# Kernel optimization log

Measured on AMD Instinct MI355X. Metric: run time of the kernel, lower is better.

Reference implementation:

```python
import jax, jax.numpy as jnp
import numpy as np

# Bernstein-basis theta coefficients for d=2 (calculate_theta2(2)),
# inv_coeff order: [x^0, x^1, x^2]
THETAS = ((3.0, -3.0, 0.75), (0.0, 3.0, -1.5), (0.0, 0.0, 0.75))
HIGH_ORDER = 2

N_NODES = 50000
N_EDGES = 800000
IN_DIM, HID_DIM, OUT_DIM = 128, 64, 2


def setup_inputs() -> dict:
    key = jax.random.key(0)
    ks = jax.random.split(key, 16)
    f32 = jnp.float32
    def w(k, shape, fan_in):
        return jax.random.normal(k, shape, dtype=f32) * (1.0 / np.sqrt(fan_in))
    return {
        "in_feat": jax.random.normal(ks[0], (N_NODES, IN_DIM), dtype=f32),
        "src": jax.random.randint(ks[1], (N_EDGES,), 0, N_NODES, dtype=jnp.int32),
        "dst": jax.random.randint(ks[2], (N_EDGES,), 0, N_NODES, dtype=jnp.int32),
        "W1": w(ks[3], (IN_DIM, HID_DIM), IN_DIM), "b1": jnp.zeros((HID_DIM,), f32),
        "W2": w(ks[4], (HID_DIM, HID_DIM), HID_DIM), "b2": jnp.zeros((HID_DIM,), f32),
        "W3": w(ks[5], (HID_DIM * 5, HID_DIM), HID_DIM * 5), "b3": jnp.zeros((HID_DIM,), f32),
        "W4": w(ks[6], (HID_DIM, OUT_DIM), HID_DIM), "b4": jnp.zeros((OUT_DIM,), f32),
        "Wg1": w(ks[7], (IN_DIM, HID_DIM), IN_DIM), "bg1": jnp.zeros((HID_DIM,), f32),
        "Wg2": w(ks[8], (HID_DIM, IN_DIM), HID_DIM), "bg2": jnp.zeros((IN_DIM,), f32),
    }


def _spmm(x, src, dst, n):
    # y[v] = sum_{(u,v) in E} x[u]   (DGL update_all(copy_u, sum))
    return jax.ops.segment_sum(x[src], dst, num_segments=n)


def reference(in_feat, src, dst, W1, b1, W2, b2, W3, b3, W4, b4, Wg1, bg1, Wg2, bg2):
    n = in_feat.shape[0]
    ones_e = jnp.ones(src.shape[0], dtype=in_feat.dtype)
    deg_in = jnp.clip(jax.ops.segment_sum(ones_e, dst, num_segments=n), 1.0)
    deg_out = jnp.clip(jax.ops.segment_sum(ones_e, src, num_segments=n), 1.0)
    din = (deg_in ** -0.5)[:, None]   # [N,1]
    dout = (deg_out ** -0.5)[:, None]

    def lap(f):
        # f - D^{-1/2} A D^{-1/2} f  (in-degree norm, as in unnLaplacian)
        return f - _spmm(f * din, src, dst, n) * din

    # MLP front-end
    h = jax.nn.relu(in_feat @ W1 + b1)
    h = jax.nn.relu(h @ W2 + b2)

    branches = []
    # BandConv branches (lin=False): theta-weighted Laplacian polynomial
    for theta in THETAS:
        f = h
        acc = theta[0] * h
        for k in range(1, len(theta)):
            f = lap(f)
            acc = acc + theta[k] * f
        branches.append(acc)
    # HighConv branches: repeated Laplacian, num_layer = 1..HIGH_ORDER
    f = h
    for j in range(HIGH_ORDER):
        f = lap(f)
        branches.append(f)

    h_final = jnp.concatenate(branches, axis=-1)  # [N, 5*hid]
    out = jax.nn.relu(h_final @ W3 + b3) @ W4 + b4  # [N, out_dim]

    # GCN branch on self-loop-free graph (same edges here): symmetric norm GraphConv
    def gconv(x, W, b):
        return _spmm(x * dout, src, dst, n) * din @ W + b
    emb = gconv(jax.nn.relu(gconv(in_feat, Wg1, bg1)), Wg2, bg2)  # [N, in_dim]

    return out, emb
```

## Files before the change

kernel.cpp:

```cpp
#include <hip/hip_runtime.h>
#include <hip/hip_bf16.h>
#include <math.h>

#define NN 50000
#define NE 800000
#define C128 128
#define CE 6250
#define NR 8
#define RNOD 6250
#define RW 3125
#define NW 25000
#define HISTB 1024
#define INITB 96
#define RB 98
#define GB 782
#define ZSB 782
#define FSG 3125

typedef _Float16 half8 __attribute__((ext_vector_type(8)));
typedef float f32x4 __attribute__((ext_vector_type(4)));
typedef unsigned short ushort4v __attribute__((ext_vector_type(4)));

static inline int cdiv(int a, int b) { return (a + b - 1) / b; }


__device__ inline size_t pack_pos(int k, int n, int K, int M) {
    int tile = n >> 4;
    int kstep = k >> 5;
    int quad = (k >> 3) & 3;
    int j = k & 7;
    int lane = (quad << 4) | (n & 15);
    return ((size_t)(tile * (K >> 5) + kstep) * 64 + lane) * 8 + j;
}

__device__ void pack_std_dev(int bx, const float* __restrict__ W, _Float16* __restrict__ Wpk,
                             int K, int M) {
    int idx = bx * 256 + threadIdx.x;
    if (idx >= K * M) return;
    int k = idx / M, n = idx % M;
    Wpk[pack_pos(k, n, K, M)] = (_Float16)W[idx];
}

__device__ void pack_wc_dev(int bx, const float* __restrict__ W3, _Float16* __restrict__ wcpk) {
    int idx = bx * 256 + threadIdx.x;
    if (idx >= 3 * 4096) return;
    int b = idx >> 12;
    int rem = idx & 4095;
    int k = rem >> 6, n = rem & 63;
    float w0 = W3[(0 * 64 + k) * 64 + n];
    float w1 = W3[(1 * 64 + k) * 64 + n];
    float w2 = W3[(2 * 64 + k) * 64 + n];
    float w3 = W3[(3 * 64 + k) * 64 + n];
    float w4 = W3[(4 * 64 + k) * 64 + n];
    float v;
    if (b == 0)      v = 3.f * w0;
    else if (b == 1) v = -3.f * w0 + 3.f * w1 + w3;
    else             v = 0.75f * w0 - 1.5f * w1 + 0.75f * w2 + w4;
    wcpk[pack_pos(b * 64 + k, n, 192, 64)] = (_Float16)v;
}

__device__ void init_dev(int bx,
                         const float* __restrict__ W2, _Float16* __restrict__ W2pk,
                         const float* __restrict__ Wg2, _Float16* __restrict__ Wg2pk,
                         const float* __restrict__ W3, _Float16* __restrict__ wcpk) {
    if (bx < 16) { pack_std_dev(bx, W2, W2pk, 64, 64); return; }
    bx -= 16;
    if (bx < 32) { pack_std_dev(bx, Wg2, Wg2pk, 64, 128); return; }
    bx -= 32;
    pack_wc_dev(bx, W3, wcpk);
}


__device__ void hist_dev(int bx, const int* __restrict__ idx, unsigned* __restrict__ H,
                         unsigned* __restrict__ cnt) {
    int c = bx & 127, r = bx >> 7;
    int tid = threadIdx.x;
    for (int j = tid; j < RW; j += 256) cnt[j] = 0;
    __syncthreads();
    int lo = r * RNOD;
    const int* p = idx + (size_t)c * CE;
    for (int i = tid; i < CE; i += 256) {
        int v = p[i] - lo;
        if ((unsigned)v < (unsigned)RNOD)
            atomicAdd(&cnt[v >> 1], 1u << ((v & 1) * 16));
    }
    __syncthreads();
    unsigned* outp = H + (size_t)c * NW + r * RW;
    for (int j = tid; j < RW; j += 256) outp[j] = cnt[j];
}

__device__ void reduce_dev(int bx, const unsigned* __restrict__ H, int* __restrict__ dgo,
                           float* __restrict__ o_rsq, float* __restrict__ o_inv,
                           float* __restrict__ o_sq) {
    int w = bx * 256 + threadIdx.x;
    if (w >= NW) return;
    unsigned slo = 0, shi = 0;
#pragma unroll 8
    for (int c = 0; c < C128; c++) {
        unsigned h = H[(size_t)c * NW + w];
        slo += h & 0xffffu; shi += h >> 16;
    }
    if (dgo) {
        dgo[2 * w]     = slo > 64u ? 64 : (int)slo;
        dgo[2 * w + 1] = shi > 64u ? 64 : (int)shi;
    }
    float f0 = (float)(slo < 1u ? 1u : slo);
    float f1 = (float)(shi < 1u ? 1u : shi);
    o_rsq[2 * w] = rsqrtf(f0); o_rsq[2 * w + 1] = rsqrtf(f1);
    if (o_inv) { o_inv[2 * w] = 1.f / f0; o_inv[2 * w + 1] = 1.f / f1; }
    if (o_sq)  { o_sq[2 * w] = sqrtf(f0); o_sq[2 * w + 1] = sqrtf(f1); }
}

__device__ void prefix_dev(int bx, const unsigned* __restrict__ HD, unsigned* __restrict__ baseD) {
    int w = bx * 256 + threadIdx.x;
    if (w >= NW) return;
    unsigned slo = 0, shi = 0;
#pragma unroll 8
    for (int c = 0; c < C128; c++) {
        unsigned b0 = slo > 64u ? 64u : slo;
        unsigned b1 = shi > 64u ? 64u : shi;
        baseD[(size_t)c * NW + w] = b0 | (b1 << 16);
        unsigned h = HD[(size_t)c * NW + w];
        slo += h & 0xffffu; shi += h >> 16;
    }
}

__device__ void scatter_dev(int bx, const int* __restrict__ src, const int* __restrict__ dst,
                            const unsigned* __restrict__ baseD,
                            unsigned short* __restrict__ colsPad,
                            unsigned* __restrict__ cnt) {
    int c = bx & 127, r = bx >> 7;
    int tid = threadIdx.x;
    const unsigned* bslice = baseD + (size_t)c * NW + r * RW;
    for (int j = tid; j < RW; j += 256) cnt[j] = bslice[j];
    __syncthreads();
    int lo = r * RNOD;
    const int* pd = dst + (size_t)c * CE;
    const int* ps = src + (size_t)c * CE;
    for (int i = tid; i < CE; i += 256) {
        int v = pd[i];
        int lv = v - lo;
        if ((unsigned)lv < (unsigned)RNOD) {
            int sh = (lv & 1) * 16;
            unsigned old = atomicAdd(&cnt[lv >> 1], 1u << sh);
            unsigned pos = (old >> sh) & 0xffffu;
            if (pos < 64u) colsPad[(size_t)v * 64 + pos] = (unsigned short)ps[i];
        }
    }
}

__device__ void zscale_dev(int bx, half8* __restrict__ pair, const float* __restrict__ dout, int N) {
    int idx = bx * 256 + threadIdx.x;
    if (idx >= N * 4) return;
    int row = idx >> 2, q = idx & 3;
    float m = dout[row];
    half8* z = pair + (size_t)row * 16 + 8 + q * 2;
    half8 a = z[0], b = z[1];
#pragma unroll
    for (int j = 0; j < 8; j++) {
        a[j] = (_Float16)((float)a[j] * m);
        b[j] = (_Float16)((float)b[j] * m);
    }
    z[0] = a; z[1] = b;
}


struct HSegs { const _Float16* p[3]; int ld[3]; };

template <int M, int K, bool OUTW, bool RSCA>
__device__ void mg_dev(int bx, HSegs A, const half8* __restrict__ Wpk,
                       const float* __restrict__ bias, int relu,
                       float* __restrict__ C,
                       _Float16* __restrict__ Ch0, const float* __restrict__ ms0,
                       const float* __restrict__ rsc,
                       const float* __restrict__ W4, const float* __restrict__ b4,
                       float* __restrict__ outp, int ldC, int N) {
    constexpr int NT = M / 16;
    constexpr int NKS = K / 32;
    int tid = threadIdx.x;
    int wave = tid >> 6, lane = tid & 63;
    int quad = lane >> 4, m = lane & 15;
    int row0 = bx * 64 + wave * 16;
    int rowA = row0 + m; if (rowA >= N) rowA = N - 1;
    _Float16 hs = (_Float16)1.f;
    if (RSCA) hs = (_Float16)rsc[rowA];
    f32x4 acc[NT];
#pragma unroll
    for (int t = 0; t < NT; t++) acc[t] = (f32x4){0.f, 0.f, 0.f, 0.f};
#pragma unroll
    for (int ks = 0; ks < NKS; ks++) {
        const _Float16* ap = A.p[ks >> 1] + (size_t)rowA * A.ld[ks >> 1] + (ks & 1) * 32 + quad * 8;
        half8 af = *(const half8*)ap;
        if (RSCA) {
#pragma unroll
            for (int j = 0; j < 8; j++) af[j] *= hs;
        }
#pragma unroll
        for (int t = 0; t < NT; t++) {
            half8 bf = Wpk[(t * NKS + ks) * 64 + lane];
            acc[t] = __builtin_amdgcn_mfma_f32_16x16x32_f16(af, bf, acc[t], 0, 0, 0);
        }
    }
    float outv[NT][4];
#pragma unroll
    for (int t = 0; t < NT; t++) {
        float bv = bias ? bias[t * 16 + m] : 0.f;
#pragma unroll
        for (int r = 0; r < 4; r++) {
            float v = acc[t][r] + bv;
            if (relu) v = fmaxf(v, 0.f);
            outv[t][r] = v;
        }
    }
    if (OUTW) {
        float w40[NT], w41[NT];
#pragma unroll
        for (int t = 0; t < NT; t++) {
            w40[t] = W4[(t * 16 + m) * 2];
            w41[t] = W4[(t * 16 + m) * 2 + 1];
        }
#pragma unroll
        for (int r = 0; r < 4; r++) {
            float p0 = 0.f, p1 = 0.f;
#pragma unroll
            for (int t = 0; t < NT; t++) {
                p0 += outv[t][r] * w40[t];
                p1 += outv[t][r] * w41[t];
            }
#pragma unroll
            for (int off = 1; off < 16; off <<= 1) {
                p0 += __shfl_xor(p0, off);
                p1 += __shfl_xor(p1, off);
            }
            int row = row0 + quad * 4 + r;
            if (m == 0 && row < N) {
                outp[(size_t)row * 2 + 0] = p0 + b4[0];
                outp[(size_t)row * 2 + 1] = p1 + b4[1];
            }
        }
    }
    if (C || Ch0) {
#pragma unroll
        for (int r = 0; r < 4; r++) {
            int row = row0 + quad * 4 + r;
            if (row >= N) continue;
            float m0 = (Ch0 && ms0) ? ms0[row] : 1.f;
#pragma unroll
            for (int t = 0; t < NT; t++) {
                size_t off = (size_t)row * ldC + t * 16 + m;
                if (C)   C[off] = outv[t][r];
                if (Ch0) Ch0[off] = (_Float16)(outv[t][r] * m0);
            }
        }
    }
}

__device__ void a15_dev(int bx, const float* __restrict__ in_feat,
                        const float* __restrict__ W1, const float* __restrict__ Wg1,
                        const float* __restrict__ b1,
                        _Float16* __restrict__ h1h, _Float16* __restrict__ zh,
                        _Float16* __restrict__ wsm, int N) {
    int tid = threadIdx.x;
    int wave = tid >> 6, lane = tid & 63;
    int quad = lane >> 4, m = lane & 15;
    int row0 = bx * 64 + wave * 16;
    int rowA = row0 + m; if (rowA >= N) rowA = N - 1;
    half8 af[4];
#pragma unroll
    for (int ks = 0; ks < 4; ks++) {
        const float* ap = in_feat + (size_t)rowA * 128 + ks * 32 + quad * 8;
        float4 u = *(const float4*)ap;
        float4 v = *(const float4*)(ap + 4);
        af[ks][0] = (_Float16)u.x; af[ks][1] = (_Float16)u.y;
        af[ks][2] = (_Float16)u.z; af[ks][3] = (_Float16)u.w;
        af[ks][4] = (_Float16)v.x; af[ks][5] = (_Float16)v.y;
        af[ks][6] = (_Float16)v.z; af[ks][7] = (_Float16)v.w;
    }
    const half8* wf = (const half8*)wsm;
    f32x4 acc[4];
    for (int i = tid; i < 8192; i += 256)
        wsm[pack_pos(i >> 6, i & 63, 128, 64)] = (_Float16)W1[i];
    __syncthreads();
#pragma unroll
    for (int t = 0; t < 4; t++) acc[t] = (f32x4){0.f, 0.f, 0.f, 0.f};
#pragma unroll
    for (int ks = 0; ks < 4; ks++)
#pragma unroll
        for (int t = 0; t < 4; t++)
            acc[t] = __builtin_amdgcn_mfma_f32_16x16x32_f16(af[ks], wf[(t * 4 + ks) * 64 + lane], acc[t], 0, 0, 0);
#pragma unroll
    for (int r = 0; r < 4; r++) {
        int row = row0 + quad * 4 + r;
        if (row >= N) continue;
#pragma unroll
        for (int t = 0; t < 4; t++)
            h1h[(size_t)row * 64 + t * 16 + m] = (_Float16)fmaxf(acc[t][r] + b1[t * 16 + m], 0.f);
    }
    __syncthreads();
    for (int i = tid; i < 8192; i += 256)
        wsm[pack_pos(i >> 6, i & 63, 128, 64)] = (_Float16)Wg1[i];
    __syncthreads();
#pragma unroll
    for (int t = 0; t < 4; t++) acc[t] = (f32x4){0.f, 0.f, 0.f, 0.f};
#pragma unroll
    for (int ks = 0; ks < 4; ks++)
#pragma unroll
        for (int t = 0; t < 4; t++)
            acc[t] = __builtin_amdgcn_mfma_f32_16x16x32_f16(af[ks], wf[(t * 4 + ks) * 64 + lane], acc[t], 0, 0, 0);
#pragma unroll
    for (int r = 0; r < 4; r++) {
        int row = row0 + quad * 4 + r;
        if (row >= N) continue;
#pragma unroll
        for (int t = 0; t < 4; t++)
            zh[(size_t)row * 128 + t * 16 + m] = (_Float16)acc[t][r];
    }
}


__launch_bounds__(256)
__global__ void k_L1(const float* __restrict__ in_feat,
                     const float* __restrict__ W1, const float* __restrict__ Wg1,
                     const float* __restrict__ b1,
                     _Float16* __restrict__ h1h, _Float16* __restrict__ zh,
                     const float* __restrict__ W2, _Float16* __restrict__ W2pk,
                     const float* __restrict__ Wg2, _Float16* __restrict__ Wg2pk,
                     const float* __restrict__ W3, _Float16* __restrict__ wcpk,
                     const int* __restrict__ src, const int* __restrict__ dst,
                     unsigned* __restrict__ HD, unsigned* __restrict__ HS, int N) {
    __shared__ _Float16 smh[8192];
    int bx = blockIdx.x;
    if (bx < GB) { a15_dev(bx, in_feat, W1, Wg1, b1, h1h, zh, smh, N); return; }
    bx -= GB;
    if (bx < INITB) { init_dev(bx, W2, W2pk, Wg2, Wg2pk, W3, wcpk); return; }
    bx -= INITB;
    if (bx < HISTB) { hist_dev(bx, dst, HD, (unsigned*)smh); return; }
    bx -= HISTB;
    hist_dev(bx, src, HS, (unsigned*)smh);
}

__launch_bounds__(256)
__global__ void k_L2(const unsigned* __restrict__ HD, const unsigned* __restrict__ HS,
                     int* __restrict__ degin, float* __restrict__ din,
                     float* __restrict__ din2, float* __restrict__ dsq,
                     float* __restrict__ dout, unsigned* __restrict__ baseD) {
    int bx = blockIdx.x;
    if (bx < RB) { reduce_dev(bx, HD, degin, din, din2, dsq); return; }
    bx -= RB;
    if (bx < RB) { reduce_dev(bx, HS, nullptr, dout, nullptr, nullptr); return; }
    bx -= RB;
    prefix_dev(bx, HD, baseD);
}

__launch_bounds__(256)
__global__ void k_L3(const int* __restrict__ src, const int* __restrict__ dst,
                     const unsigned* __restrict__ baseD, unsigned short* __restrict__ colsPad,
                     const _Float16* __restrict__ h1h, const half8* __restrict__ W2pk,
                     const float* __restrict__ b2, _Float16* __restrict__ pair0h,
                     const float* __restrict__ din,
                     half8* __restrict__ pair0v, const float* __restrict__ dout, int N) {
    __shared__ unsigned cnt[RW];
    int bx = blockIdx.x;
    if (bx < HISTB) { scatter_dev(bx, src, dst, baseD, colsPad, cnt); return; }
    bx -= HISTB;
    if (bx < GB) {
        HSegs A;
        A.p[0] = h1h; A.ld[0] = 64;
        A.p[1] = nullptr; A.ld[1] = 0;
        A.p[2] = nullptr; A.ld[2] = 0;
        mg_dev<64, 64, false, false>(bx, A, W2pk, b2, 1, nullptr, pair0h, din,
                                     nullptr, nullptr, nullptr, nullptr, 128, N);
        return;
    }
    bx -= GB;
    zscale_dev(bx, pair0v, dout, N);
}


struct FSP {
    const half8* xp;
    half8* uOut; int uld;
    half8* zOut; int zld;
    const float* din2;
    const float* zrs1;
    const float* bgz;
    const float* zrs2;
    int zrelu;
};

__launch_bounds__(256)
__global__ void k_FS(FSP P, const unsigned short* __restrict__ colsPad,
                     const int* __restrict__ deg, int N) {
    int g = blockIdx.x;
    int tid = threadIdx.x;
    int wave = tid >> 6, lane = tid & 63;
    int grp = lane >> 4, c = lane & 15;
    int row = g * 16 + wave * 4 + grp;
    if (row >= N) return;
    int dg = deg[row];
    const unsigned short* cp = colsPad + (size_t)row * 64;
    float acc[8];
#pragma unroll
    for (int j = 0; j < 8; j++) acc[j] = 0.f;
    int e = 0;
    for (; e + 7 < dg; e += 8) {
        ushort4v sa = *(const ushort4v*)(cp + e);
        ushort4v sb = *(const ushort4v*)(cp + e + 4);
        half8 v0 = P.xp[(size_t)sa.x * 16 + c];
        half8 v1 = P.xp[(size_t)sa.y * 16 + c];
        half8 v2 = P.xp[(size_t)sa.z * 16 + c];
        half8 v3 = P.xp[(size_t)sa.w * 16 + c];
        half8 v4 = P.xp[(size_t)sb.x * 16 + c];
        half8 v5 = P.xp[(size_t)sb.y * 16 + c];
        half8 v6 = P.xp[(size_t)sb.z * 16 + c];
        half8 v7 = P.xp[(size_t)sb.w * 16 + c];
#pragma unroll
        for (int j = 0; j < 8; j++) {
            acc[j] += (float)v0[j] + (float)v1[j] + (float)v2[j] + (float)v3[j]
                    + (float)v4[j] + (float)v5[j] + (float)v6[j] + (float)v7[j];
        }
    }
    for (; e + 3 < dg; e += 4) {
        ushort4v ss = *(const ushort4v*)(cp + e);
        half8 v0 = P.xp[(size_t)ss.x * 16 + c];
        half8 v1 = P.xp[(size_t)ss.y * 16 + c];
        half8 v2 = P.xp[(size_t)ss.z * 16 + c];
        half8 v3 = P.xp[(size_t)ss.w * 16 + c];
#pragma unroll
        for (int j = 0; j < 8; j++)
            acc[j] += (float)v0[j] + (float)v1[j] + (float)v2[j] + (float)v3[j];
    }
    for (; e < dg; e++) {
        int s = cp[e];
        half8 v = P.xp[(size_t)s * 16 + c];
#pragma unroll
        for (int j = 0; j < 8; j++) acc[j] += (float)v[j];
    }
    half8 h;
    if (c < 8) {
        float d = P.din2[row];
        half8 f = P.xp[(size_t)row * 16 + c];
#pragma unroll
        for (int j = 0; j < 8; j++)
            h[j] = (_Float16)((float)f[j] - acc[j] * d);
        P.uOut[(size_t)row * P.uld + c] = h;
    } else {
        float s1 = P.zrs1[row];
#pragma unroll
        for (int j = 0; j < 8; j++) acc[j] *= s1;
        if (P.bgz) {
            const float* bb = P.bgz + (c - 8) * 8;
#pragma unroll
            for (int j = 0; j < 8; j++) acc[j] += bb[j];
        }
        if (P.zrelu) {
#pragma unroll
            for (int j = 0; j < 8; j++) acc[j] = fmaxf(acc[j], 0.f);
        }
        float s2 = P.zrs2 ? P.zrs2[row] : 1.f;
#pragma unroll
        for (int j = 0; j < 8; j++) h[j] = (_Float16)(acc[j] * s2);
        P.zOut[(size_t)row * P.zld + (c - 8)] = h;
    }
}

__launch_bounds__(256)
__global__ void k_F3(const _Float16* __restrict__ pair0, const _Float16* __restrict__ pair1,
                     const _Float16* __restrict__ u2h, const half8* __restrict__ wcpk,
                     const float* __restrict__ b3, const float* __restrict__ dsq,
                     const float* __restrict__ W4, const float* __restrict__ b4,
                     float* __restrict__ outp,
                     const _Float16* __restrict__ sgh, const half8* __restrict__ Wg2pk,
                     const float* __restrict__ bg2, float* __restrict__ emb, int N) {
    int bx = blockIdx.x;
    if (bx < GB) {
        HSegs A;
        A.p[0] = pair0; A.ld[0] = 128;
        A.p[1] = pair1; A.ld[1] = 128;
        A.p[2] = u2h;   A.ld[2] = 64;
        mg_dev<64, 192, true, true>(bx, A, wcpk, b3, 1, nullptr, nullptr, nullptr,
                                    dsq, W4, b4, outp, 64, N);
        return;
    }
    bx -= GB;
    HSegs A;
    A.p[0] = sgh; A.ld[0] = 64;
    A.p[1] = nullptr; A.ld[1] = 0;
    A.p[2] = nullptr; A.ld[2] = 0;
    mg_dev<128, 64, false, false>(bx, A, Wg2pk, bg2, 0, emb, nullptr, nullptr,
                                  nullptr, nullptr, nullptr, nullptr, 128, N);
}

extern "C" void kernel_launch(void* const* d_in, const int* in_sizes, int n_in,
                              void* d_out, int out_size, void* d_ws, size_t ws_size,
                              hipStream_t stream) {
    const int N = NN;
    const float* in_feat = (const float*)d_in[0];
    const int* src = (const int*)d_in[1];
    const int* dst = (const int*)d_in[2];
    const float* W1 = (const float*)d_in[3];
    const float* b1 = (const float*)d_in[4];
    const float* W2 = (const float*)d_in[5];
    const float* b2 = (const float*)d_in[6];
    const float* W3 = (const float*)d_in[7];
    const float* b3 = (const float*)d_in[8];
    const float* W4 = (const float*)d_in[9];
    const float* b4 = (const float*)d_in[10];
    const float* Wg1 = (const float*)d_in[11];
    const float* bg1 = (const float*)d_in[12];
    const float* Wg2 = (const float*)d_in[13];
    const float* bg2 = (const float*)d_in[14];

    float* out = (float*)d_out;
    float* emb = out + (size_t)N * 2;

    float* fw = (float*)d_ws;
    float* din  = fw;
    float* din2 = din + N;
    float* dsq  = din2 + N;
    float* dout = dsq + N;
    int* degin  = (int*)(dout + N);
    unsigned short* colsPad = (unsigned short*)(degin + N);
    unsigned* HD   = (unsigned*)(colsPad + (size_t)64 * N);
    unsigned* HS   = HD + (size_t)C128 * NW;
    unsigned* baseD = HS + (size_t)C128 * NW;
    _Float16* hp = (_Float16*)(baseD + (size_t)C128 * NW);
    _Float16* h1h   = hp;
    _Float16* pair0 = h1h + (size_t)64 * N;
    _Float16* pair1 = pair0 + (size_t)128 * N;
    _Float16* u2h   = pair1 + (size_t)128 * N;
    _Float16* sgh   = u2h + (size_t)64 * N;
    _Float16* W2pk  = sgh + (size_t)64 * N;
    _Float16* Wg2pk = W2pk + 4096;
    _Float16* wcpk  = Wg2pk + 8192;

    k_L1<<<GB + INITB + 2 * HISTB, 256, 0, stream>>>(in_feat, W1, Wg1, b1,
        h1h, pair0 + 64, W2, W2pk, Wg2, Wg2pk, W3, wcpk, src, dst, HD, HS, N);

    k_L2<<<3 * RB, 256, 0, stream>>>(HD, HS, degin, din, din2, dsq, dout, baseD);

    k_L3<<<HISTB + GB + ZSB, 256, 0, stream>>>(src, dst, baseD, colsPad,
        h1h, (const half8*)W2pk, b2, pair0, din, (half8*)pair0, dout, N);

    FSP p;
    p = {(const half8*)pair0, (half8*)pair1, 16, (half8*)pair1 + 8, 16,
         din2, din, bg1, dout, 1};
    k_FS<<<FSG, 256, 0, stream>>>(p, colsPad, degin, N);

    p = {(const half8*)pair1, (half8*)u2h, 8, (half8*)sgh, 8,
         din2, din, nullptr, nullptr, 0};
    k_FS<<<FSG, 256, 0, stream>>>(p, colsPad, degin, N);

    k_F3<<<2 * GB, 256, 0, stream>>>(pair0, pair1, u2h, (const half8*)wcpk, b3, dsq,
        W4, b4, out, sgh, (const half8*)Wg2pk, bg2, emb, N);
}
```

Baseline: 248.3 us.

## Vectorize edge index loads and merge in-degree reduce into prefix pass

Histogram and scatter loops now read edge indices as int2 pairs, halving load instructions. The separate in-degree reduction pass, which re-read the full HD histogram, is merged into the prefix pass, so HD is scanned once instead of twice. Weight-packing blocks move from the first launch into the second, freeing the first kernel for histogram and GEMM work. The int2 loads assume the per-chunk base pointers are 8-byte aligned, which holds because CE is even.

```diff
diff --git a/kernel.cpp b/kernel.cpp
--- a/kernel.cpp
+++ b/kernel.cpp
@@ -78,20 +78,22 @@
     for (int j = tid; j < RW; j += 256) cnt[j] = 0;
     __syncthreads();
     int lo = r * RNOD;
-    const int* p = idx + (size_t)c * CE;
-    for (int i = tid; i < CE; i += 256) {
-        int v = p[i] - lo;
-        if ((unsigned)v < (unsigned)RNOD)
-            atomicAdd(&cnt[v >> 1], 1u << ((v & 1) * 16));
+    const int2* p2 = (const int2*)(idx + (size_t)c * CE);
+    for (int i = tid; i < CE / 2; i += 256) {
+        int2 e = p2[i];
+        int v0 = e.x - lo, v1 = e.y - lo;
+        if ((unsigned)v0 < (unsigned)RNOD)
+            atomicAdd(&cnt[v0 >> 1], 1u << ((v0 & 1) * 16));
+        if ((unsigned)v1 < (unsigned)RNOD)
+            atomicAdd(&cnt[v1 >> 1], 1u << ((v1 & 1) * 16));
     }
     __syncthreads();
     unsigned* outp = H + (size_t)c * NW + r * RW;
     for (int j = tid; j < RW; j += 256) outp[j] = cnt[j];
 }
 
-__device__ void reduce_dev(int bx, const unsigned* __restrict__ H, int* __restrict__ dgo,
-                           float* __restrict__ o_rsq, float* __restrict__ o_inv,
-                           float* __restrict__ o_sq) {
+__device__ void reduce_dev(int bx, const unsigned* __restrict__ H,
+                           float* __restrict__ o_rsq) {
     int w = bx * 256 + threadIdx.x;
     if (w >= NW) return;
     unsigned slo = 0, shi = 0;
@@ -100,18 +102,15 @@
         unsigned h = H[(size_t)c * NW + w];
         slo += h & 0xffffu; shi += h >> 16;
     }
-    if (dgo) {
-        dgo[2 * w]     = slo > 64u ? 64 : (int)slo;
-        dgo[2 * w + 1] = shi > 64u ? 64 : (int)shi;
-    }
     float f0 = (float)(slo < 1u ? 1u : slo);
     float f1 = (float)(shi < 1u ? 1u : shi);
     o_rsq[2 * w] = rsqrtf(f0); o_rsq[2 * w + 1] = rsqrtf(f1);
-    if (o_inv) { o_inv[2 * w] = 1.f / f0; o_inv[2 * w + 1] = 1.f / f1; }
-    if (o_sq)  { o_sq[2 * w] = sqrtf(f0); o_sq[2 * w + 1] = sqrtf(f1); }
-}
-
-__device__ void prefix_dev(int bx, const unsigned* __restrict__ HD, unsigned* __restrict__ baseD) {
+}
+
+__device__ void prefnorm_dev(int bx, const unsigned* __restrict__ HD,
+                             unsigned* __restrict__ baseD,
+                             int* __restrict__ dgo, float* __restrict__ o_rsq,
+                             float* __restrict__ o_inv, float* __restrict__ o_sq) {
     int w = bx * 256 + threadIdx.x;
     if (w >= NW) return;
     unsigned slo = 0, shi = 0;
@@ -123,6 +122,13 @@
         unsigned h = HD[(size_t)c * NW + w];
         slo += h & 0xffffu; shi += h >> 16;
     }
+    dgo[2 * w]     = slo > 64u ? 64 : (int)slo;
+    dgo[2 * w + 1] = shi > 64u ? 64 : (int)shi;
+    float f0 = (float)(slo < 1u ? 1u : slo);
+    float f1 = (float)(shi < 1u ? 1u : shi);
+    o_rsq[2 * w] = rsqrtf(f0); o_rsq[2 * w + 1] = rsqrtf(f1);
+    o_inv[2 * w] = 1.f / f0;   o_inv[2 * w + 1] = 1.f / f1;
+    o_sq[2 * w] = sqrtf(f0);   o_sq[2 * w + 1] = sqrtf(f1);
 }
 
 __device__ void scatter_dev(int bx, const int* __restrict__ src, const int* __restrict__ dst,
@@ -135,16 +141,24 @@
     for (int j = tid; j < RW; j += 256) cnt[j] = bslice[j];
     __syncthreads();
     int lo = r * RNOD;
-    const int* pd = dst + (size_t)c * CE;
-    const int* ps = src + (size_t)c * CE;
-    for (int i = tid; i < CE; i += 256) {
-        int v = pd[i];
-        int lv = v - lo;
-        if ((unsigned)lv < (unsigned)RNOD) {
-            int sh = (lv & 1) * 16;
-            unsigned old = atomicAdd(&cnt[lv >> 1], 1u << sh);
+    const int2* pd2 = (const int2*)(dst + (size_t)c * CE);
+    const int2* ps2 = (const int2*)(src + (size_t)c * CE);
+    for (int i = tid; i < CE / 2; i += 256) {
+        int2 ed = pd2[i];
+        int2 es = ps2[i];
+        int lv0 = ed.x - lo;
+        if ((unsigned)lv0 < (unsigned)RNOD) {
+            int sh = (lv0 & 1) * 16;
+            unsigned old = atomicAdd(&cnt[lv0 >> 1], 1u << sh);
             unsigned pos = (old >> sh) & 0xffffu;
-            if (pos < 64u) colsPad[(size_t)v * 64 + pos] = (unsigned short)ps[i];
+            if (pos < 64u) colsPad[(size_t)ed.x * 64 + pos] = (unsigned short)es.x;
+        }
+        int lv1 = ed.y - lo;
+        if ((unsigned)lv1 < (unsigned)RNOD) {
+            int sh = (lv1 & 1) * 16;
+            unsigned old = atomicAdd(&cnt[lv1 >> 1], 1u << sh);
+            unsigned pos = (old >> sh) & 0xffffu;
+            if (pos < 64u) colsPad[(size_t)ed.y * 64 + pos] = (unsigned short)es.y;
         }
     }
 }
@@ -323,17 +337,12 @@
                      const float* __restrict__ W1, const float* __restrict__ Wg1,
                      const float* __restrict__ b1,
                      _Float16* __restrict__ h1h, _Float16* __restrict__ zh,
-                     const float* __restrict__ W2, _Float16* __restrict__ W2pk,
-                     const float* __restrict__ Wg2, _Float16* __restrict__ Wg2pk,
-                     const float* __restrict__ W3, _Float16* __restrict__ wcpk,
                      const int* __restrict__ src, const int* __restrict__ dst,
                      unsigned* __restrict__ HD, unsigned* __restrict__ HS, int N) {
     __shared__ _Float16 smh[8192];
     int bx = blockIdx.x;
     if (bx < GB) { a15_dev(bx, in_feat, W1, Wg1, b1, h1h, zh, smh, N); return; }
     bx -= GB;
-    if (bx < INITB) { init_dev(bx, W2, W2pk, Wg2, Wg2pk, W3, wcpk); return; }
-    bx -= INITB;
     if (bx < HISTB) { hist_dev(bx, dst, HD, (unsigned*)smh); return; }
     bx -= HISTB;
     hist_dev(bx, src, HS, (unsigned*)smh);
@@ -343,13 +352,16 @@
 __global__ void k_L2(const unsigned* __restrict__ HD, const unsigned* __restrict__ HS,
                      int* __restrict__ degin, float* __restrict__ din,
                      float* __restrict__ din2, float* __restrict__ dsq,
-                     float* __restrict__ dout, unsigned* __restrict__ baseD) {
+                     float* __restrict__ dout, unsigned* __restrict__ baseD,
+                     const float* __restrict__ W2, _Float16* __restrict__ W2pk,
+                     const float* __restrict__ Wg2, _Float16* __restrict__ Wg2pk,
+                     const float* __restrict__ W3, _Float16* __restrict__ wcpk) {
     int bx = blockIdx.x;
-    if (bx < RB) { reduce_dev(bx, HD, degin, din, din2, dsq); return; }
+    if (bx < RB) { reduce_dev(bx, HS, dout); return; }
     bx -= RB;
-    if (bx < RB) { reduce_dev(bx, HS, nullptr, dout, nullptr, nullptr); return; }
+    if (bx < RB) { prefnorm_dev(bx, HD, baseD, degin, din, din2, dsq); return; }
     bx -= RB;
-    prefix_dev(bx, HD, baseD);
+    init_dev(bx, W2, W2pk, Wg2, Wg2pk, W3, wcpk);
 }
 
 __launch_bounds__(256)
@@ -534,10 +546,11 @@
     _Float16* Wg2pk = W2pk + 4096;
     _Float16* wcpk  = Wg2pk + 8192;
 
-    k_L1<<<GB + INITB + 2 * HISTB, 256, 0, stream>>>(in_feat, W1, Wg1, b1,
-        h1h, pair0 + 64, W2, W2pk, Wg2, Wg2pk, W3, wcpk, src, dst, HD, HS, N);
-
-    k_L2<<<3 * RB, 256, 0, stream>>>(HD, HS, degin, din, din2, dsq, dout, baseD);
+    k_L1<<<GB + 2 * HISTB, 256, 0, stream>>>(in_feat, W1, Wg1, b1,
+        h1h, pair0 + 64, src, dst, HD, HS, N);
+
+    k_L2<<<2 * RB + INITB, 256, 0, stream>>>(HD, HS, degin, din, din2, dsq, dout, baseD,
+        W2, W2pk, Wg2, Wg2pk, W3, wcpk);
 
     k_L3<<<HISTB + GB + ZSB, 256, 0, stream>>>(src, dst, baseD, colsPad,
         h1h, (const half8*)W2pk, b2, pair0, din, (half8*)pair0, dout, N);
```

Result: faster. 240.0 us (median of 2 runs) (-3.4%).
